# Optimization experiments

Hardware: AMD Instinct MI355X
Metric: run time of the kernel (lower is better)

Reference implementation:

```python
import jax, jax.numpy as jnp
import numpy as np

B, C, H, W = 2, 48, 128, 256
HEADS = 3
EPS_LN = 1e-6
EPS_NRM = 1e-12


def _conv(x, w, b, padding=0, dilation=1, groups=1):
    # x: NCHW, w: OIHW
    out = jax.lax.conv_general_dilated(
        x, w, window_strides=(1, 1),
        padding=[(padding, padding), (padding, padding)],
        rhs_dilation=(dilation, dilation),
        feature_group_count=groups,
        dimension_numbers=('NCHW', 'OIHW', 'NCHW'))
    return out + b[None, :, None, None]


def _ln2d(x, w, b):
    # LayerNorm over channel dim per pixel (NAFNet-style LayerNorm2d)
    mu = x.mean(axis=1, keepdims=True)
    var = ((x - mu) ** 2).mean(axis=1, keepdims=True)
    return (x - mu) / jnp.sqrt(var + EPS_LN) * w[None, :, None, None] + b[None, :, None, None]


def _l2norm(x):
    # F.normalize(dim=-1): x / max(||x||_2, eps)
    n = jnp.sqrt((x * x).sum(-1, keepdims=True))
    return x / jnp.maximum(n, EPS_NRM)


def setup_inputs() -> dict:
    key = jax.random.key(0)
    ks = iter(jax.random.split(key, 40))
    def nrm(shape, s=0.02):
        return jax.random.normal(next(ks), shape, jnp.float32) * s
    d = {
        'x_l': jax.random.normal(next(ks), (B, C, H, W), jnp.float32),
        'x_r': jax.random.normal(next(ks), (B, C, H, W), jnp.float32),
        'ln1_w': jnp.ones((C,), jnp.float32), 'ln1_b': jnp.zeros((C,), jnp.float32),
        'ln2_w': jnp.ones((C,), jnp.float32), 'ln2_b': jnp.zeros((C,), jnp.float32),
        'qkv_l_w': nrm((3 * C, C, 1, 1)), 'qkv_l_b': jnp.zeros((3 * C,), jnp.float32),
        'qkv_r_w': nrm((3 * C, C, 1, 1)), 'qkv_r_b': jnp.zeros((3 * C,), jnp.float32),
        'dw_l_w': nrm((3 * C, 1, 3, 3)), 'dw_l_b': jnp.zeros((3 * C,), jnp.float32),
        'dw_r_w': nrm((3 * C, 1, 3, 3)), 'dw_r_b': jnp.zeros((3 * C,), jnp.float32),
        'dil0_w': nrm((2 * C, 2 * C, 3, 3)), 'dil0_b': jnp.zeros((2 * C,), jnp.float32),
        'dil1_w': nrm((2 * C, 2 * C, 3, 3)), 'dil1_b': jnp.zeros((2 * C,), jnp.float32),
        'dil2_w': nrm((2 * C, 2 * C, 3, 3)), 'dil2_b': jnp.zeros((2 * C,), jnp.float32),
        'convQ_w': nrm((C, 6 * C, 1, 1)), 'convQ_b': jnp.zeros((C,), jnp.float32),
        'conv1_w': nrm((C, C, 1, 1)), 'conv1_b': jnp.zeros((C,), jnp.float32),
        'conv2_w': nrm((C, C, 1, 1)), 'conv2_b': jnp.zeros((C,), jnp.float32),
        'temperature': jnp.ones((HEADS, 1, 1), jnp.float32),
    }
    return d


def reference(x_l, x_r, ln1_w, ln1_b, ln2_w, ln2_b,
              qkv_l_w, qkv_l_b, qkv_r_w, qkv_r_b,
              dw_l_w, dw_l_b, dw_r_w, dw_r_b,
              dil0_w, dil0_b, dil1_w, dil1_b, dil2_w, dil2_b,
              convQ_w, convQ_b, conv1_w, conv1_b, conv2_w, conv2_b,
              temperature):
    b, c, h, w = x_l.shape
    hw = h * w
    ch = c // HEADS  # channels per head

    norm_l = _ln2d(x_l, ln1_w, ln1_b)
    norm_r = _ln2d(x_r, ln2_w, ln2_b)

    qkvl = _conv(_conv(norm_l, qkv_l_w, qkv_l_b), dw_l_w, dw_l_b, padding=1, groups=3 * c)
    qkvr = _conv(_conv(norm_r, qkv_r_w, qkv_r_b), dw_r_w, dw_r_b, padding=1, groups=3 * c)
    Q_l, K_l, V_l = jnp.split(qkvl, 3, axis=1)
    Q_r, K_r, V_r = jnp.split(qkvr, 3, axis=1)

    Q = jnp.concatenate((Q_l, Q_r), axis=1)  # [b, 2c, h, w]
    Q = jnp.concatenate((
        _conv(Q, dil0_w, dil0_b, padding=2, dilation=2),
        _conv(Q, dil1_w, dil1_b, padding=4, dilation=4),
        _conv(Q, dil2_w, dil2_b, padding=6, dilation=6)), axis=1)  # [b, 6c, h, w]
    Q = _conv(Q, convQ_w, convQ_b)  # [b, c, h, w]

    def heads(t):
        return t.reshape(b, HEADS, ch, hw)

    Q = _l2norm(heads(Q))
    K_l = _l2norm(heads(K_l))
    K_r = _l2norm(heads(K_r))
    V_l = heads(V_l)
    V_r = heads(V_r)

    # channel attention: [b, head, ch, ch]
    A_r2l = jax.nn.softmax(jnp.einsum('bhcn,bhdn->bhcd', Q, K_r) * temperature, axis=-1)
    A_l2r = jax.nn.softmax(jnp.einsum('bhcn,bhdn->bhcd', Q, K_l) * temperature, axis=-1)

    F_l = jnp.einsum('bhcd,bhdn->bhcn', A_r2l, V_l).reshape(b, c, h, w)
    F_r = jnp.einsum('bhcd,bhdn->bhcn', A_l2r, V_r).reshape(b, c, h, w)

    F_l = _conv(F_l, conv1_w, conv1_b)
    F_r = _conv(F_r, conv2_w, conv2_b)
    return (x_l + F_l, x_r + F_r)
```

## Files before the change

### kernel.cpp

```cpp
#include <hip/hip_runtime.h>
#include <hip/hip_bf16.h>

typedef __hip_bfloat16 bf16;
typedef __attribute__((ext_vector_type(8))) short short8;
typedef __attribute__((ext_vector_type(4))) float f32x4;

constexpr int IMG_H = 128;
constexpr int IMG_W = 256;
constexpr int HW    = IMG_H * IMG_W;
constexpr int BB    = 2;
constexpr int CC    = 48;
constexpr int C3    = 144;
constexpr int XPW   = 268;
constexpr int XOFF  = 6;

constexpr int WO_QKVL_W = 0;
constexpr int WO_QKVR_W = 6912;
constexpr int WO_DWL_W  = 13824;
constexpr int WO_DWR_W  = 15120;
constexpr int WO_C1_W   = 16416;
constexpr int WO_C2_W   = 18720;
constexpr int WO_QKVL_B = 21024;
constexpr int WO_QKVR_B = 21168;
constexpr int WO_DWL_B  = 21312;
constexpr int WO_DWR_B  = 21456;
constexpr int WO_C1_B   = 21600;
constexpr int WO_C2_B   = 21648;
constexpr int WO_LN1W   = 21696;
constexpr int WO_LN1B   = 21744;
constexpr int WO_LN2W   = 21792;
constexpr int WO_LN2B   = 21840;
constexpr int WO_TEMP   = 21888;
constexpr int WO_WQ     = 21952;
constexpr int WO_D0W    = 35776;
constexpr int WO_D1W    = 118720;
constexpr int WO_D2W    = 201664;
constexpr int WO_BQ     = 284608;
constexpr int WO_B0     = 284656;
constexpr int WO_B1     = 284752;
constexpr int WO_B2     = 284848;
constexpr int WO_WPACK  = 284944;
constexpr int WO_EFFB   = 409360;
constexpr int WO_NQ     = 409424;
constexpr int WO_NKL    = 409520;
constexpr int WO_NKR    = 409616;
constexpr int WO_AR2L   = 409712;
constexpr int WO_AL2R   = 411248;
constexpr int WO_M1     = 412800;
constexpr int WO_M2     = 417408;
constexpr int WO_WQP    = 422016;
constexpr int WO_PART   = 431232;

constexpr size_t ACT_BASE_BYTES = 2118144;

constexpr size_t A_P  = 0;
constexpr size_t A_Q1 = 9437184;
constexpr size_t A_Q2 = 18874368;
constexpr size_t A_QC = 28311552;

struct PrepArgs {
  const void* src[25];
  int dst[25];
  int n[25];
};

__device__ __forceinline__ bool probe_bf16(const void* ln1w) {
  return ((const unsigned short*)ln1w)[0] == 0x3F80;
}

__global__ __launch_bounds__(256) void prep_k(PrepArgs a, float* __restrict__ wsf) {
  bool isb = probe_bf16(a.src[12]);
  int t = blockIdx.y;
  int i = blockIdx.x * 256 + threadIdx.x;
  if (i < a.n[t]) {
    float v = isb ? __bfloat162float(((const bf16*)a.src[t])[i])
                  : ((const float*)a.src[t])[i];
    wsf[a.dst[t] + i] = v;
  }
}

__global__ __launch_bounds__(256) void effw2_k(const float* __restrict__ wsf,
                                               bf16* __restrict__ wpack) {
  int d  = blockIdx.x / 96;
  int ci = blockIdx.x % 96;
  __shared__ float wds[864];
  __shared__ float wqs[48 * 97];
  const int wdb = (d == 0) ? WO_D0W : (d == 1) ? WO_D1W : WO_D2W;
  for (int idx = threadIdx.x; idx < 864; idx += 256) {
    int m = idx / 9, tt = idx % 9;
    wds[idx] = wsf[wdb + (m * 96 + ci) * 9 + tt];
  }
  for (int idx = threadIdx.x; idx < 4608; idx += 256) {
    int co = idx / 96, m = idx % 96;
    wqs[co * 97 + m] = wsf[WO_WQ + co * 288 + d * 96 + m];
  }
  __syncthreads();
  int tco = threadIdx.x;
  if (tco < 432) {
    int t = tco / 48, co = tco % 48;
    float s = 0.f;
#pragma unroll 8
    for (int m = 0; m < 96; ++m) s += wqs[co * 97 + m] * wds[m * 9 + t];
    int trow = t / 3, dxi = t % 3;
    int ti = (trow == 0) ? (2 - d) * 3 + dxi
           : (trow == 1) ? 9 + d * 3 + dxi
                         : 18 + d * 3 + dxi;
    int kc = ci >> 5, j = ci & 7;
    int L = ((ci & 31) >> 3) * 16 + (co & 15);
    int nt = co >> 4;
    int f = (ti * 3 + kc) * 3 + nt;
    wpack[(size_t)f * 512 + L * 8 + j] = __float2bfloat16(s);
  }
}

__global__ __launch_bounds__(64) void effb_k(const float* __restrict__ wsf,
                                             float* __restrict__ effb) {
  int co = threadIdx.x;
  if (co >= 48) return;
  float s = wsf[WO_BQ + co];
  for (int m = 0; m < 96; ++m) {
    s += wsf[WO_WQ + co * 288 + m]       * wsf[WO_B0 + m];
    s += wsf[WO_WQ + co * 288 + 96 + m]  * wsf[WO_B1 + m];
    s += wsf[WO_WQ + co * 288 + 192 + m] * wsf[WO_B2 + m];
  }
  effb[co] = s;
}

__global__ __launch_bounds__(256) void wqp_k(const float* __restrict__ wsf,
                                             bf16* __restrict__ wqp) {
  int idx = blockIdx.x * 256 + threadIdx.x;
  if (idx >= 18432) return;
  int side = idx / 9216;
  int rem = idx % 9216;
  int nt = rem / 1024;
  int kt = (rem / 512) % 2;
  int e  = rem % 512;
  int L = e >> 3, j = e & 7;
  int o = nt * 16 + (L & 15);
  int kp = kt * 32 + (L >> 4) * 8 + j;
  int g = kp >> 4, r = kp & 15;
  float val = 0.f;
  if (r < 12) {
    int c = g * 12 + r;
    val = wsf[(side ? WO_QKVR_W : WO_QKVL_W) + o * 48 + c];
  }
  wqp[idx] = __float2bfloat16(val);
}

__global__ __launch_bounds__(256) void lnqkv_k(
    const void* __restrict__ x, const void* __restrict__ probe,
    const float* __restrict__ lnw, const float* __restrict__ lnb,
    const bf16* __restrict__ wqp_side, const float* __restrict__ qb,
    bf16* __restrict__ pre) {
  __shared__ __align__(16) unsigned char LDSU[21504 + 18432];
  bf16* XNs = (bf16*)LDSU;
  float2* red = (float2*)(LDSU + 9216);
  bf16* Cs = (bf16*)LDSU;
  bf16* W = (bf16*)(LDSU + 21504);
  int tid = threadIdx.x;
  for (int i = tid; i < 1152; i += 256)
    ((uint4*)W)[i] = ((const uint4*)wqp_side)[i];

  int px = tid & 63;
  int w = tid >> 6;
  int p = blockIdx.x * 64 + px;
  int b = p >> 15;
  int pix = p & (HW - 1);
  size_t base = (size_t)b * CC * HW + pix;
  float v[12];
  if (probe_bf16(probe)) {
    const bf16* xp = (const bf16*)x + base;
#pragma unroll
    for (int c = 0; c < 12; ++c)
      v[c] = __bfloat162float(xp[(size_t)(w * 12 + c) * HW]);
  } else {
    const float* xp = (const float*)x + base;
#pragma unroll
    for (int c = 0; c < 12; ++c) v[c] = xp[(size_t)(w * 12 + c) * HW];
  }
  float s = 0.f, s2 = 0.f;
#pragma unroll
  for (int c = 0; c < 12; ++c) { s += v[c]; s2 += v[c] * v[c]; }
  red[w * 64 + px] = make_float2(s, s2);
  __syncthreads();
  float S = 0.f, S2 = 0.f;
#pragma unroll
  for (int i = 0; i < 4; ++i) {
    float2 r2 = red[i * 64 + px];
    S += r2.x; S2 += r2.y;
  }
  float mu = S * (1.f / 48.f);
  float var = S2 * (1.f / 48.f) - mu * mu;
  float rs = rsqrtf(var + 1e-6f);
  bf16 o16[16];
#pragma unroll
  for (int c = 0; c < 12; ++c)
    o16[c] = __float2bfloat16((v[c] - mu) * rs * lnw[w * 12 + c] + lnb[w * 12 + c]);
#pragma unroll
  for (int c = 12; c < 16; ++c) o16[c] = __float2bfloat16(0.f);
  *(uint4*)(XNs + px * 72 + w * 16) = *(uint4*)(o16);
  *(uint4*)(XNs + px * 72 + w * 16 + 8) = *(uint4*)(o16 + 8);
  __syncthreads();

  int L = tid & 63;
  int lo = L & 15, hi = L >> 4;
  const bf16* arow = XNs + (size_t)(w * 16 + lo) * 72 + hi * 8;
  short8 a0 = *(const short8*)(arow);
  short8 a1 = *(const short8*)(arow + 32);
  __syncthreads();
#pragma unroll
  for (int nt = 0; nt < 9; ++nt) {
    float bvv = qb[nt * 16 + lo];
    f32x4 acc = {bvv, bvv, bvv, bvv};
    acc = __builtin_amdgcn_mfma_f32_16x16x32_bf16(
        a0, *(const short8*)(W + (nt * 2 + 0) * 512 + L * 8), acc, 0, 0, 0);
    acc = __builtin_amdgcn_mfma_f32_16x16x32_bf16(
        a1, *(const short8*)(W + (nt * 2 + 1) * 512 + L * 8), acc, 0, 0, 0);
#pragma unroll
    for (int r = 0; r < 4; ++r)
      Cs[(nt * 16 + lo) * 66 + w * 16 + hi * 4 + r] = __float2bfloat16(acc[r]);
  }
  __syncthreads();
  int pix0 = (blockIdx.x * 64) & (HW - 1);
#pragma unroll
  for (int pass = 0; pass < 18; ++pass) {
    int o = pass * 8 + (tid >> 5);
    int px2 = (tid & 31) * 2;
    bf16 t2[2];
    t2[0] = Cs[o * 66 + px2];
    t2[1] = Cs[o * 66 + px2 + 1];
    *(unsigned*)(pre + ((size_t)(b * C3 + o)) * HW + pix0 + px2) = *(unsigned*)t2;
  }
}

__global__ __launch_bounds__(256) void dw_k(
    const bf16* __restrict__ in, const float* __restrict__ w9,
    const float* __restrict__ bias, bf16* __restrict__ out) {
  int gid = blockIdx.x;
  int yt = gid & 15;
  int c = (gid >> 4) % C3;
  int b = gid / (16 * C3);
  int ry = threadIdx.x >> 5, xi = threadIdx.x & 31;
  int y = yt * 8 + ry;
  int x0 = xi * 8;
  const bf16* base = in + ((size_t)(b * C3 + c)) * HW;
  float wv[9];
#pragma unroll
  for (int t = 0; t < 9; ++t) wv[t] = w9[c * 9 + t];
  float bz = bias[c];
  float acc[8];
#pragma unroll
  for (int i = 0; i < 8; ++i) acc[i] = bz;
#pragma unroll
  for (int ky = 0; ky < 3; ++ky) {
    int yy = y + ky - 1;
    if ((unsigned)yy >= (unsigned)IMG_H) continue;
    const bf16* row = base + yy * IMG_W + x0;
    uint4 m = *(const uint4*)(row);
    float f[10];
    f[0] = (x0 > 0) ? __bfloat162float(row[-1]) : 0.f;
    f[9] = (x0 + 8 < IMG_W) ? __bfloat162float(row[8]) : 0.f;
    f[1] = __uint_as_float(m.x << 16);
    f[2] = __uint_as_float(m.x & 0xFFFF0000u);
    f[3] = __uint_as_float(m.y << 16);
    f[4] = __uint_as_float(m.y & 0xFFFF0000u);
    f[5] = __uint_as_float(m.z << 16);
    f[6] = __uint_as_float(m.z & 0xFFFF0000u);
    f[7] = __uint_as_float(m.w << 16);
    f[8] = __uint_as_float(m.w & 0xFFFF0000u);
    float w0 = wv[ky * 3], w1 = wv[ky * 3 + 1], w2 = wv[ky * 3 + 2];
#pragma unroll
    for (int i = 0; i < 8; ++i)
      acc[i] += w0 * f[i] + w1 * f[i + 1] + w2 * f[i + 2];
  }
  bf16 o[8];
#pragma unroll
  for (int i = 0; i < 8; ++i) o[i] = __float2bfloat16(acc[i]);
  *(uint4*)(out + ((size_t)(b * C3 + c)) * HW + y * IMG_W + x0) = *(uint4*)o;
}

__global__ __launch_bounds__(256) void qc_k(const bf16* __restrict__ q1,
                                            const bf16* __restrict__ q2,
                                            bf16* __restrict__ qc) {
  int b = blockIdx.x >> 7;
  int y = blockIdx.x & 127;
  int half = blockIdx.y;
  int tid = threadIdx.x;
  int x0 = half * 128;
  int px = tid & 127;
  int cig = tid >> 7;
  __shared__ __align__(16) bf16 T[128][100];
#pragma unroll 8
  for (int k = 0; k < 48; ++k) {
    int ci = cig * 48 + k;
    const bf16* src = (ci < 48)
        ? q1 + (((size_t)(b * C3 + ci)) * IMG_H + y) * IMG_W
        : q2 + (((size_t)(b * C3 + ci - 48)) * IMG_H + y) * IMG_W;
    T[px][ci] = src[x0 + px];
  }
  __syncthreads();
  size_t rowbase = ((size_t)(b * IMG_H + y)) * XPW * 96 + (size_t)half * 12864;
#pragma unroll 1
  for (int i = 0; i < 13; ++i) {
    int e4 = i * 256 + tid;
    if (e4 >= 3216) break;
    int e = e4 * 4;
    int xp = (e + half * 12864) / 96;
    int ci = (e + half * 12864) % 96;
    int x = xp - XOFF;
    uint2 val;
    if ((unsigned)x < (unsigned)IMG_W) {
      val = *(const uint2*)(&T[x - x0][ci]);
    } else {
      val.x = 0u; val.y = 0u;
    }
    *(uint2*)(qc + rowbase + e) = val;
  }
}

__global__ __launch_bounds__(128) void dil_mfma_k(
    const bf16* __restrict__ qc, const bf16* __restrict__ wp,
    const float* __restrict__ effb, bf16* __restrict__ qh) {
  __shared__ __align__(16) unsigned char LDSU[8768];
  bf16* Wb = (bf16*)LDSU;
  float* Cs = (float*)LDSU;
  int bid = blockIdx.x;
  int xcd = bid & 7;
  int slot = bid >> 3;
  int y = xcd * 16 + (slot & 15);
  int rest = slot >> 4;
  int xt = rest & 1;
  int b = (rest >> 1) & 1;
  int cg = rest >> 2;
  int tid = threadIdx.x;
  int L = tid & 63;
  int w = tid >> 6;
  int lo = L & 15, hi = L >> 4;
  int x0 = xt * 128;

  f32x4 acc[4];
  {
    float bv = effb[cg * 16 + lo];
#pragma unroll
    for (int s = 0; s < 4; ++s) acc[s] = {bv, bv, bv, bv};
  }
  const size_t abase =
      ((size_t)(b * IMG_H + y) * XPW + XOFF + x0 + w * 64 + lo) * 96 + hi * 8;

  for (int t = tid; t < 192; t += 128) {
    int kc = t >> 6, e = t & 63;
    ((uint4*)(Wb))[kc * 64 + e] =
        *((const uint4*)(wp + ((size_t)(0 * 3 + kc) * 3 + cg) * 512) + e);
  }
  __syncthreads();

#pragma unroll 1
  for (int ti = 0; ti < 27; ++ti) {
    if (ti + 1 < 27) {
      int tn = ti + 1;
      for (int t = tid; t < 192; t += 128) {
        int kc = t >> 6, e = t & 63;
        ((uint4*)(Wb + (tn & 1) * 1536))[kc * 64 + e] =
            *((const uint4*)(wp + ((size_t)(tn * 3 + kc) * 3 + cg) * 512) + e);
      }
    }
    int g = ti / 3, dxi = ti - g * 3;
    int D = (g < 3) ? (6 - 2 * g) : (g < 6) ? (2 * (g - 2)) : (2 * (g - 5));
    int dy = (g < 3) ? -D : (g < 6) ? 0 : D;
    int dx = (dxi - 1) * D;
    if ((unsigned)(y + dy) < (unsigned)IMG_H) {
      const bf16* wb = Wb + (ti & 1) * 1536;
      const bf16* ap = qc + abase + ((long)dy * XPW + dx) * 96;
#pragma unroll
      for (int kc = 0; kc < 3; ++kc) {
        short8 wv = *(const short8*)(wb + kc * 512 + L * 8);
#pragma unroll
        for (int s = 0; s < 4; ++s) {
          short8 a = *(const short8*)(ap + kc * 32 + s * 1536);
          acc[s] = __builtin_amdgcn_mfma_f32_16x16x32_bf16(a, wv, acc[s], 0, 0, 0);
        }
      }
    }
    __syncthreads();
  }

#pragma unroll
  for (int s = 0; s < 4; ++s)
#pragma unroll
    for (int r = 0; r < 4; ++r)
      Cs[lo * 137 + w * 64 + s * 16 + hi * 4 + r] = acc[s][r];
  __syncthreads();
#pragma unroll
  for (int p = 0; p < 2; ++p) {
    int e = (p * 128 + tid) * 8;
    int co = e >> 7;
    int px = e & 127;
    const float* srcp = &Cs[co * 137 + px];
    bf16 tmp[8];
#pragma unroll
    for (int i2 = 0; i2 < 8; ++i2) tmp[i2] = __float2bfloat16(srcp[i2]);
    *(uint4*)(qh + (((size_t)(b * CC + cg * 16 + co)) * IMG_H + y) * IMG_W +
              x0 + px) = *(uint4*)tmp;
  }
}

__device__ __forceinline__ float wave_sum(float v) {
#pragma unroll
  for (int off = 32; off > 0; off >>= 1) v += __shfl_down(v, off, 64);
  return v;
}

__device__ __forceinline__ float blo(unsigned u) {
  return __uint_as_float(u << 16);
}
__device__ __forceinline__ float bhi(unsigned u) {
  return __uint_as_float(u & 0xFFFF0000u);
}

__global__ __launch_bounds__(256) void rownorm_k(
    const bf16* __restrict__ qh, const bf16* __restrict__ qkvl,
    const bf16* __restrict__ qkvr, float* __restrict__ nq,
    float* __restrict__ nkl, float* __restrict__ nkr) {
  int id = blockIdx.x;
  int which = id / 96;
  int rid = id % 96;
  int b = rid / 48;
  int c = rid % 48;
  const bf16* ptr = (which == 0) ? qh + ((size_t)(b * CC + c)) * HW
                  : (which == 1) ? qkvl + ((size_t)(b * C3 + 48 + c)) * HW
                                 : qkvr + ((size_t)(b * C3 + 48 + c)) * HW;
  float s = 0.f;
#pragma unroll 2
  for (int it = 0; it < 16; ++it) {
    int n0 = (it * 256 + threadIdx.x) * 8;
    uint4 u = *(const uint4*)(ptr + n0);
    float a0 = blo(u.x), a1 = bhi(u.x), a2 = blo(u.y), a3 = bhi(u.y);
    float a4 = blo(u.z), a5 = bhi(u.z), a6 = blo(u.w), a7 = bhi(u.w);
    s += a0 * a0 + a1 * a1 + a2 * a2 + a3 * a3 + a4 * a4 + a5 * a5 +
         a6 * a6 + a7 * a7;
  }
  s = wave_sum(s);
  __shared__ float red[4];
  if ((threadIdx.x & 63) == 0) red[threadIdx.x >> 6] = s;
  __syncthreads();
  if (threadIdx.x == 0) {
    float tot = red[0] + red[1] + red[2] + red[3];
    float* dst = (which == 0) ? nq : (which == 1) ? nkl : nkr;
    dst[rid] = tot;
  }
}

__global__ __launch_bounds__(256) void logits_mfma_k(
    const bf16* __restrict__ qh, const bf16* __restrict__ qkvl,
    const bf16* __restrict__ qkvr, float* __restrict__ part) {
  int abh = blockIdx.x;
  int chunk = blockIdx.y;
  int a = abh / 6;
  int b = (abh / 3) % 2;
  int h = abh % 3;
  int tid = threadIdx.x;
  int L = tid & 63, w = tid >> 6;
  int lo = L & 15, hi = L >> 4;
  const bf16* qrow = qh + ((size_t)(b * CC + h * 16 + lo)) * HW;
  const bf16* krow =
      ((a == 0) ? qkvr : qkvl) + ((size_t)(b * C3 + 48 + h * 16 + lo)) * HW;
  int px0 = chunk * 1024 + w * 256 + hi * 8;
  f32x4 acc = {0.f, 0.f, 0.f, 0.f};
#pragma unroll
  for (int s = 0; s < 8; ++s) {
    short8 av = *(const short8*)(qrow + px0 + s * 32);
    short8 bv = *(const short8*)(krow + px0 + s * 32);
    acc = __builtin_amdgcn_mfma_f32_16x16x32_bf16(av, bv, acc, 0, 0, 0);
  }
  __shared__ float red[4][256];
#pragma unroll
  for (int r = 0; r < 4; ++r) red[w][(hi * 4 + r) * 16 + lo] = acc[r];
  __syncthreads();
  float sum = red[0][tid] + red[1][tid] + red[2][tid] + red[3][tid];
  part[((size_t)abh * 32 + chunk) * 256 + tid] = sum;
}

__global__ __launch_bounds__(256) void logits_red_k(
    const float* __restrict__ part, const float* __restrict__ nq,
    const float* __restrict__ nkl, const float* __restrict__ nkr,
    const float* __restrict__ temp, float* __restrict__ logr2l,
    float* __restrict__ logl2r) {
  int abh = blockIdx.x;
  int a = abh / 6, b = (abh / 3) % 2, h = abh % 3;
  int t = threadIdx.x;
  int i = t >> 4, j = t & 15;
  float s = 0.f;
  const float* p = part + (size_t)abh * 32 * 256 + t;
#pragma unroll 8
  for (int c = 0; c < 32; ++c) s += p[c * 256];
  float qn = fmaxf(sqrtf(nq[b * 48 + h * 16 + i]), 1e-12f);
  float kn = fmaxf(sqrtf(((a == 0) ? nkr : nkl)[b * 48 + h * 16 + j]), 1e-12f);
  float val = s / (qn * kn) * temp[h];
  ((a == 0) ? logr2l : logl2r)[b * 768 + h * 256 + i * 16 + j] = val;
}

__global__ __launch_bounds__(256) void softmaxM_k(float* __restrict__ wsf) {
  int tid = threadIdx.x;
  __shared__ float A1[1536], A2[1536];
  if (tid < 192) {
    const float* p = wsf + ((tid < 96) ? WO_AR2L : WO_AL2R) + (tid % 96) * 16;
    float* dst = ((tid < 96) ? A1 : A2) + (tid % 96) * 16;
    float m = -1e30f;
#pragma unroll
    for (int j = 0; j < 16; ++j) m = fmaxf(m, p[j]);
    float s = 0.f;
    float e[16];
#pragma unroll
    for (int j = 0; j < 16; ++j) {
      e[j] = expf(p[j] - m);
      s += e[j];
    }
    float inv = 1.f / s;
#pragma unroll
    for (int j = 0; j < 16; ++j) dst[j] = e[j] * inv;
  }
  __syncthreads();
#pragma unroll 1
  for (int idx = tid; idx < 4608; idx += 256) {
    int b = idx / 2304;
    int r = idx % 2304;
    int o = r / 48;
    int cp = r % 48;
    int h = cp >> 4, j = cp & 15;
    const float* a1 = &A1[((b * 3 + h) * 16) * 16 + j];
    const float* a2 = &A2[((b * 3 + h) * 16) * 16 + j];
    float s1 = 0.f, s2 = 0.f;
#pragma unroll
    for (int i = 0; i < 16; ++i) {
      s1 += wsf[WO_C1_W + o * 48 + h * 16 + i] * a1[i * 16];
      s2 += wsf[WO_C2_W + o * 48 + h * 16 + i] * a2[i * 16];
    }
    wsf[WO_M1 + idx] = s1;
    wsf[WO_M2 + idx] = s2;
  }
}

__global__ __launch_bounds__(256) void attn_out2_k(
    const bf16* __restrict__ q1, const bf16* __restrict__ q2,
    const void* __restrict__ x1, const void* __restrict__ x2,
    const void* __restrict__ probe, const float* __restrict__ Mall,
    const float* __restrict__ cball, void* __restrict__ out) {
  int side = blockIdx.z;
  const bf16* qkv = side ? q2 : q1;
  const void* x = side ? x2 : x1;
  const float* M = Mall + side * 4608;
  const float* cb = cball + side * 48;
  int tid = threadIdx.x;
  int p = blockIdx.x * 256 + tid;
  int b = __builtin_amdgcn_readfirstlane(p >> 15);
  int pix = p & (HW - 1);
  int o0 = blockIdx.y * 16;
  bool isb = probe_bf16(probe);

  float v[CC];
  const bf16* vb = qkv + ((size_t)(b * C3 + 96)) * HW + pix;
#pragma unroll
  for (int c = 0; c < CC; ++c) v[c] = __bfloat162float(vb[(size_t)c * HW]);

  const float* Mb = M + b * 2304;
  size_t base = (size_t)b * CC * HW + pix;
  float res[16];
#pragma unroll 2
  for (int o = 0; o < 16; ++o) {
    float acc = cb[o0 + o];
    const float* mrow = Mb + (o0 + o) * 48;
#pragma unroll
    for (int c = 0; c < CC; ++c) acc += mrow[c] * v[c];
    res[o] = acc;
  }
  size_t obase = (size_t)side * BB * CC * HW + base + (size_t)o0 * HW;
  if (isb) {
    const bf16* xp = (const bf16*)x + base + (size_t)o0 * HW;
    bf16* op = (bf16*)out + obase;
#pragma unroll
    for (int o = 0; o < 16; ++o)
      op[(size_t)o * HW] =
          __float2bfloat16(res[o] + __bfloat162float(xp[(size_t)o * HW]));
  } else {
    const float* xp = (const float*)x + base + (size_t)o0 * HW;
    float* op = (float*)out + obase;
#pragma unroll
    for (int o = 0; o < 16; ++o) op[(size_t)o * HW] = res[o] + xp[(size_t)o * HW];
  }
}

extern "C" void kernel_launch(void* const* d_in, const int* in_sizes, int n_in,
                              void* d_out, int out_size, void* d_ws, size_t ws_size,
                              hipStream_t stream) {
  (void)in_sizes; (void)n_in; (void)out_size; (void)ws_size;
  const void* x_l = d_in[0];
  const void* x_r = d_in[1];
  const void* probe = d_in[2];
  float* wsf = (float*)d_ws;
  bf16* wpack = (bf16*)(wsf + WO_WPACK);
  bf16* wqp = (bf16*)(wsf + WO_WQP);
  bf16* act = (bf16*)((char*)d_ws + ACT_BASE_BYTES);
  bf16* P  = act + A_P;
  bf16* Q1 = act + A_Q1;
  bf16* Q2 = act + A_Q2;
  bf16* QC = act + A_QC;
  bf16* qh = P;

  PrepArgs pa;
  const int srcIdx[25] = {6, 8, 10, 12, 22, 24, 7, 9, 11, 13, 23, 25,
                          2, 3, 4, 5, 26, 20, 14, 16, 18, 21, 15, 17, 19};
  const int dstOff[25] = {WO_QKVL_W, WO_QKVR_W, WO_DWL_W, WO_DWR_W, WO_C1_W, WO_C2_W,
                          WO_QKVL_B, WO_QKVR_B, WO_DWL_B, WO_DWR_B, WO_C1_B, WO_C2_B,
                          WO_LN1W, WO_LN1B, WO_LN2W, WO_LN2B, WO_TEMP,
                          WO_WQ, WO_D0W, WO_D1W, WO_D2W, WO_BQ, WO_B0, WO_B1, WO_B2};
  const int ns[25] = {6912, 6912, 1296, 1296, 2304, 2304, 144, 144, 144, 144,
                      48, 48, 48, 48, 48, 48, 3,
                      13824, 82944, 82944, 82944, 48, 96, 96, 96};
  for (int i = 0; i < 25; ++i) {
    pa.src[i] = d_in[srcIdx[i]];
    pa.dst[i] = dstOff[i];
    pa.n[i] = ns[i];
  }
  prep_k<<<dim3(324, 25), 256, 0, stream>>>(pa, wsf);

  effw2_k<<<288, 256, 0, stream>>>(wsf, wpack);
  effb_k<<<1, 64, 0, stream>>>(wsf, wsf + WO_EFFB);
  wqp_k<<<72, 256, 0, stream>>>(wsf, wqp);

  lnqkv_k<<<1024, 256, 0, stream>>>(x_l, probe, wsf + WO_LN1W, wsf + WO_LN1B,
                                    wqp, wsf + WO_QKVL_B, P);
  dw_k<<<BB * C3 * 16, 256, 0, stream>>>(P, wsf + WO_DWL_W, wsf + WO_DWL_B, Q1);
  lnqkv_k<<<1024, 256, 0, stream>>>(x_r, probe, wsf + WO_LN2W, wsf + WO_LN2B,
                                    wqp + 9216, wsf + WO_QKVR_B, P);
  dw_k<<<BB * C3 * 16, 256, 0, stream>>>(P, wsf + WO_DWR_W, wsf + WO_DWR_B, Q2);

  qc_k<<<dim3(BB * IMG_H, 2), 256, 0, stream>>>(Q1, Q2, QC);

  dil_mfma_k<<<1536, 128, 0, stream>>>(QC, wpack, wsf + WO_EFFB, qh);

  rownorm_k<<<288, 256, 0, stream>>>(qh, Q1, Q2, wsf + WO_NQ,
                                     wsf + WO_NKL, wsf + WO_NKR);
  logits_mfma_k<<<dim3(12, 32), 256, 0, stream>>>(qh, Q1, Q2, wsf + WO_PART);
  logits_red_k<<<12, 256, 0, stream>>>(wsf + WO_PART, wsf + WO_NQ,
                                       wsf + WO_NKL, wsf + WO_NKR,
                                       wsf + WO_TEMP, wsf + WO_AR2L,
                                       wsf + WO_AL2R);
  softmaxM_k<<<1, 256, 0, stream>>>(wsf);

  attn_out2_k<<<dim3(256, 3, 2), 256, 0, stream>>>(
      Q1, Q2, x_l, x_r, probe, wsf + WO_M1, wsf + WO_C1_B, d_out);
}
```

Measured before the change: 315.2 us.

## Retile dilated conv MFMA kernel to compute all output channels per block

The dilated-conv MFMA kernel now has each block compute all 48 output channels for a 64-pixel strip, instead of 16 channels for a 128-pixel strip. Each A fragment loaded from global memory is reused across three output-channel tiles, which removes the 3x re-read of the activation input across channel groups. The block grows to 256 threads with 1024 blocks, and the weight tile staged in LDS per tap becomes 3x larger. The cost is more LDS per block, fewer accumulators per wave, and narrower output stores.

New measurement: 280.0 us. 11.2% less time.

```diff
diff --git a/kernel.cpp b/kernel.cpp
--- a/kernel.cpp
+++ b/kernel.cpp
@@ -318,10 +318,10 @@
   }
 }
 
-__global__ __launch_bounds__(128) void dil_mfma_k(
+__global__ __launch_bounds__(256) void dil_mfma_k(
     const bf16* __restrict__ qc, const bf16* __restrict__ wp,
     const float* __restrict__ effb, bf16* __restrict__ qh) {
-  __shared__ __align__(16) unsigned char LDSU[8768];
+  __shared__ __align__(16) unsigned char LDSU[18432];
   bf16* Wb = (bf16*)LDSU;
   float* Cs = (float*)LDSU;
   int bid = blockIdx.x;
@@ -329,55 +329,56 @@
   int slot = bid >> 3;
   int y = xcd * 16 + (slot & 15);
   int rest = slot >> 4;
-  int xt = rest & 1;
-  int b = (rest >> 1) & 1;
-  int cg = rest >> 2;
+  int xt = rest & 3;
+  int b = rest >> 2;
+  int x0 = xt * 64;
   int tid = threadIdx.x;
   int L = tid & 63;
   int w = tid >> 6;
   int lo = L & 15, hi = L >> 4;
-  int x0 = xt * 128;
-
-  f32x4 acc[4];
+
+  f32x4 acc[3];
+#pragma unroll
+  for (int nt = 0; nt < 3; ++nt) {
+    float bv = effb[nt * 16 + lo];
+    acc[nt] = {bv, bv, bv, bv};
+  }
+  const size_t abase =
+      ((size_t)(b * IMG_H + y) * XPW + XOFF + x0 + w * 16 + lo) * 96 + hi * 8;
+
   {
-    float bv = effb[cg * 16 + lo];
-#pragma unroll
-    for (int s = 0; s < 4; ++s) acc[s] = {bv, bv, bv, bv};
-  }
-  const size_t abase =
-      ((size_t)(b * IMG_H + y) * XPW + XOFF + x0 + w * 64 + lo) * 96 + hi * 8;
-
-  for (int t = tid; t < 192; t += 128) {
-    int kc = t >> 6, e = t & 63;
-    ((uint4*)(Wb))[kc * 64 + e] =
-        *((const uint4*)(wp + ((size_t)(0 * 3 + kc) * 3 + cg) * 512) + e);
+    const uint4* src = (const uint4*)(wp);
+    uint4* dst = (uint4*)(Wb);
+    dst[tid] = src[tid];
+    dst[tid + 256] = src[tid + 256];
+    if (tid < 64) dst[tid + 512] = src[tid + 512];
   }
   __syncthreads();
 
 #pragma unroll 1
   for (int ti = 0; ti < 27; ++ti) {
     if (ti + 1 < 27) {
-      int tn = ti + 1;
-      for (int t = tid; t < 192; t += 128) {
-        int kc = t >> 6, e = t & 63;
-        ((uint4*)(Wb + (tn & 1) * 1536))[kc * 64 + e] =
-            *((const uint4*)(wp + ((size_t)(tn * 3 + kc) * 3 + cg) * 512) + e);
-      }
+      const uint4* src = (const uint4*)(wp + (ti + 1) * 4608);
+      uint4* dst = (uint4*)(Wb + ((ti + 1) & 1) * 4608);
+      dst[tid] = src[tid];
+      dst[tid + 256] = src[tid + 256];
+      if (tid < 64) dst[tid + 512] = src[tid + 512];
     }
     int g = ti / 3, dxi = ti - g * 3;
     int D = (g < 3) ? (6 - 2 * g) : (g < 6) ? (2 * (g - 2)) : (2 * (g - 5));
     int dy = (g < 3) ? -D : (g < 6) ? 0 : D;
     int dx = (dxi - 1) * D;
     if ((unsigned)(y + dy) < (unsigned)IMG_H) {
-      const bf16* wb = Wb + (ti & 1) * 1536;
+      const bf16* wb = Wb + (ti & 1) * 4608;
       const bf16* ap = qc + abase + ((long)dy * XPW + dx) * 96;
 #pragma unroll
       for (int kc = 0; kc < 3; ++kc) {
-        short8 wv = *(const short8*)(wb + kc * 512 + L * 8);
-#pragma unroll
-        for (int s = 0; s < 4; ++s) {
-          short8 a = *(const short8*)(ap + kc * 32 + s * 1536);
-          acc[s] = __builtin_amdgcn_mfma_f32_16x16x32_bf16(a, wv, acc[s], 0, 0, 0);
+        short8 a = *(const short8*)(ap + kc * 32);
+        const bf16* wk = wb + kc * 3 * 512 + L * 8;
+#pragma unroll
+        for (int nt = 0; nt < 3; ++nt) {
+          acc[nt] = __builtin_amdgcn_mfma_f32_16x16x32_bf16(
+              a, *(const short8*)(wk + nt * 512), acc[nt], 0, 0, 0);
         }
       }
     }
@@ -385,22 +386,24 @@
   }
 
 #pragma unroll
-  for (int s = 0; s < 4; ++s)
+  for (int nt = 0; nt < 3; ++nt)
 #pragma unroll
     for (int r = 0; r < 4; ++r)
-      Cs[lo * 137 + w * 64 + s * 16 + hi * 4 + r] = acc[s][r];
-  __syncthreads();
-#pragma unroll
-  for (int p = 0; p < 2; ++p) {
-    int e = (p * 128 + tid) * 8;
-    int co = e >> 7;
-    int px = e & 127;
-    const float* srcp = &Cs[co * 137 + px];
-    bf16 tmp[8];
-#pragma unroll
-    for (int i2 = 0; i2 < 8; ++i2) tmp[i2] = __float2bfloat16(srcp[i2]);
-    *(uint4*)(qh + (((size_t)(b * CC + cg * 16 + co)) * IMG_H + y) * IMG_W +
-              x0 + px) = *(uint4*)tmp;
+      Cs[(nt * 16 + lo) * 68 + w * 16 + hi * 4 + r] = acc[nt][r];
+  __syncthreads();
+#pragma unroll
+  for (int i = 0; i < 3; ++i) {
+    int e4 = i * 256 + tid;
+    int co = e4 >> 4;
+    int px4 = (e4 & 15) * 4;
+    const float* srcp = &Cs[co * 68 + px4];
+    bf16 tmp[4];
+    tmp[0] = __float2bfloat16(srcp[0]);
+    tmp[1] = __float2bfloat16(srcp[1]);
+    tmp[2] = __float2bfloat16(srcp[2]);
+    tmp[3] = __float2bfloat16(srcp[3]);
+    *(uint2*)(qh + (((size_t)(b * CC + co)) * IMG_H + y) * IMG_W + x0 + px4) =
+        *(uint2*)tmp;
   }
 }
 
@@ -636,7 +639,7 @@
 
   qc_k<<<dim3(BB * IMG_H, 2), 256, 0, stream>>>(Q1, Q2, QC);
 
-  dil_mfma_k<<<1536, 128, 0, stream>>>(QC, wpack, wsf + WO_EFFB, qh);
+  dil_mfma_k<<<1024, 256, 0, stream>>>(QC, wpack, wsf + WO_EFFB, qh);
 
   rownorm_k<<<288, 256, 0, stream>>>(qh, Q1, Q2, wsf + WO_NQ,
                                      wsf + WO_NKL, wsf + WO_NKR);
```
